# Kernel tuning notes

Measured on AMD Instinct MI355X. Metric: run time of the kernel, lower is better.

Reference implementation:

```python
import jax, jax.numpy as jnp
import numpy as np

# per-position segment id for seq_len=16: slices [0:1],[1:6],[6:9],[9:10],[10:16]
SEG = np.array([0] + [1]*5 + [2]*3 + [3] + [4]*6, dtype=np.int32)
HEAD_DIM = 3
NUM_HEADS = 2


def setup_inputs() -> dict:
    key = jax.random.key(0)
    ks = jax.random.split(key, 9)
    B = 262144
    s = 1.0 / np.sqrt(6.0)  # torch Linear init scale
    return {
        "x": jax.random.normal(ks[0], (B, 16, 6), dtype=jnp.float32),
        "Wq": jax.random.uniform(ks[1], (5, 6, 6), jnp.float32, -s, s),
        "bq": jax.random.uniform(ks[2], (5, 6), jnp.float32, -s, s),
        "Wk": jax.random.uniform(ks[3], (5, 6, 6), jnp.float32, -s, s),
        "bk": jax.random.uniform(ks[4], (5, 6), jnp.float32, -s, s),
        "Wv": jax.random.uniform(ks[5], (5, 6, 6), jnp.float32, -s, s),
        "bv": jax.random.uniform(ks[6], (5, 6), jnp.float32, -s, s),
        "Wo": jax.random.uniform(ks[7], (6, 6), jnp.float32, -s, s),
        "bo": jax.random.uniform(ks[8], (6,), jnp.float32, -s, s),
    }


def reference(x, Wq, bq, Wk, bk, Wv, bv, Wo, bo):
    B, S, D = x.shape  # S=16, D=6
    seg = jnp.asarray(SEG)

    def seg_proj(W, b):
        # torch Linear: y = x @ W.T + b; gather per-position segment weights
        return jnp.einsum('bsd,sod->bso', x, W[seg]) + b[seg]

    def heads(t):
        return t.reshape(B, S, NUM_HEADS, HEAD_DIM).transpose(0, 2, 1, 3)

    Q = heads(seg_proj(Wq, bq))  # [B,H,S,hd]
    K = heads(seg_proj(Wk, bk))
    V = heads(seg_proj(Wv, bv))

    scores = jnp.einsum('bhqd,bhkd->bhqk', Q, K) / jnp.sqrt(jnp.float32(HEAD_DIM))
    attn = jax.nn.softmax(scores, axis=-1)
    ctx = jnp.einsum('bhqk,bhkd->bhqd', attn, V)
    ctx = ctx.transpose(0, 2, 1, 3).reshape(B, S, D)
    return ctx @ Wo.T + bo
```

## Files before the change

### kernel.cpp

```cpp
#include <hip/hip_runtime.h>

#define SCALE 0.57735026918962576f

#define OFF_WQ 0
#define OFF_BQ 260
#define OFF_WK 300
#define OFF_BK 560
#define OFF_WV 600
#define OFF_BV 860
#define OFF_WO 900
#define OFF_BO 948
#define OFF_K  956
#define OFF_V  3068
#define GSTRIDE 132
#define LDS_FLOATS 5180

__global__ __launch_bounds__(256) void attn_seg_kernel(
    const float* __restrict__ x,
    const float* __restrict__ Wq, const float* __restrict__ bq,
    const float* __restrict__ Wk, const float* __restrict__ bk,
    const float* __restrict__ Wv, const float* __restrict__ bv,
    const float* __restrict__ Wo, const float* __restrict__ bo,
    float* __restrict__ out, int total)
{
    __shared__ __align__(16) float lds[LDS_FLOATS];
    const int t = threadIdx.x;

    if (t < 180) {
        unsigned sg = (unsigned)t / 36u, r = (unsigned)t - sg * 36u;
        unsigned o = r / 6u, d = r - o * 6u;
        int dst = (int)(sg * 52u + o * 8u + d);
        lds[OFF_WQ + dst] = Wq[t];
        lds[OFF_WK + dst] = Wk[t];
        lds[OFF_WV + dst] = Wv[t];
    }
    if (t < 30) {
        unsigned sg = (unsigned)t / 6u, o = (unsigned)t - sg * 6u;
        lds[OFF_BQ + sg * 8u + o] = bq[t];
        lds[OFF_BK + sg * 8u + o] = bk[t];
        lds[OFF_BV + sg * 8u + o] = bv[t];
    }
    if (t < 36) {
        unsigned o = (unsigned)t / 6u, d = (unsigned)t - o * 6u;
        lds[OFF_WO + o * 8u + d] = Wo[t];
    }
    if (t < 6) lds[OFF_BO + t] = bo[t];

    const int g = t >> 4;
    const int s = t & 15;
    const int seg = (s == 0) ? 0 : (s < 6) ? 1 : (s < 9) ? 2 : (s == 9) ? 3 : 4;

    const int pos = blockIdx.x * 256 + t;
    const bool valid = pos < total;
    float x0=0.f,x1=0.f,x2=0.f,x3=0.f,x4=0.f,x5=0.f;
    if (valid) {
        const float* xp = x + (size_t)pos * 6;
        float2 a = *(const float2*)(xp);
        float2 b = *(const float2*)(xp + 2);
        float2 c = *(const float2*)(xp + 4);
        x0=a.x; x1=a.y; x2=b.x; x3=b.y; x4=c.x; x5=c.y;
    }

    __syncthreads();

    float q[6], kk[6], vv[6];
    {
        const float* W = &lds[OFF_WQ + seg * 52];
        float4 b4 = *(const float4*)&lds[OFF_BQ + seg * 8];
        float2 b2 = *(const float2*)&lds[OFF_BQ + seg * 8 + 4];
        float bb[6] = {b4.x, b4.y, b4.z, b4.w, b2.x, b2.y};
        #pragma unroll
        for (int o = 0; o < 6; o++) {
            float4 w4 = *(const float4*)(W + o * 8);
            float2 w2 = *(const float2*)(W + o * 8 + 4);
            q[o] = bb[o] + x0*w4.x + x1*w4.y + x2*w4.z + x3*w4.w + x4*w2.x + x5*w2.y;
        }
    }
    {
        const float* W = &lds[OFF_WK + seg * 52];
        float4 b4 = *(const float4*)&lds[OFF_BK + seg * 8];
        float2 b2 = *(const float2*)&lds[OFF_BK + seg * 8 + 4];
        float bb[6] = {b4.x, b4.y, b4.z, b4.w, b2.x, b2.y};
        #pragma unroll
        for (int o = 0; o < 6; o++) {
            float4 w4 = *(const float4*)(W + o * 8);
            float2 w2 = *(const float2*)(W + o * 8 + 4);
            kk[o] = bb[o] + x0*w4.x + x1*w4.y + x2*w4.z + x3*w4.w + x4*w2.x + x5*w2.y;
        }
    }
    {
        const float* W = &lds[OFF_WV + seg * 52];
        float4 b4 = *(const float4*)&lds[OFF_BV + seg * 8];
        float2 b2 = *(const float2*)&lds[OFF_BV + seg * 8 + 4];
        float bb[6] = {b4.x, b4.y, b4.z, b4.w, b2.x, b2.y};
        #pragma unroll
        for (int o = 0; o < 6; o++) {
            float4 w4 = *(const float4*)(W + o * 8);
            float2 w2 = *(const float2*)(W + o * 8 + 4);
            vv[o] = bb[o] + x0*w4.x + x1*w4.y + x2*w4.z + x3*w4.w + x4*w2.x + x5*w2.y;
        }
    }

    {
        float* Kd = &lds[OFF_K + g * GSTRIDE + s * 8];
        *(float4*)Kd       = make_float4(kk[0], kk[1], kk[2], kk[3]);
        *(float2*)(Kd + 4) = make_float2(kk[4], kk[5]);
        float* Vd = &lds[OFF_V + g * GSTRIDE + s * 8];
        *(float4*)Vd       = make_float4(vv[0], vv[1], vv[2], vv[3]);
        *(float2*)(Vd + 4) = make_float2(vv[4], vv[5]);
    }

    __syncthreads();

    #pragma unroll
    for (int i = 0; i < 6; i++) q[i] *= SCALE;

    float sc0[16], sc1[16];
    {
        const float* Kb = &lds[OFF_K + g * GSTRIDE];
        #pragma unroll
        for (int k = 0; k < 16; k++) {
            float4 a = *(const float4*)(Kb + k * 8);
            float2 b = *(const float2*)(Kb + k * 8 + 4);
            sc0[k] = q[0]*a.x + q[1]*a.y + q[2]*a.z;
            sc1[k] = q[3]*a.w + q[4]*b.x + q[5]*b.y;
        }
    }

    float m0 = sc0[0], m1 = sc1[0];
    #pragma unroll
    for (int k = 1; k < 16; k++) { m0 = fmaxf(m0, sc0[k]); m1 = fmaxf(m1, sc1[k]); }
    float sum0 = 0.f, sum1 = 0.f;
    #pragma unroll
    for (int k = 0; k < 16; k++) {
        float e0 = __expf(sc0[k] - m0); sc0[k] = e0; sum0 += e0;
        float e1 = __expf(sc1[k] - m1); sc1[k] = e1; sum1 += e1;
    }
    const float inv0 = __builtin_amdgcn_rcpf(sum0);
    const float inv1 = __builtin_amdgcn_rcpf(sum1);

    float c0=0.f,c1=0.f,c2=0.f,c3=0.f,c4=0.f,c5=0.f;
    {
        const float* Vb = &lds[OFF_V + g * GSTRIDE];
        #pragma unroll
        for (int k = 0; k < 16; k++) {
            float4 a = *(const float4*)(Vb + k * 8);
            float2 b = *(const float2*)(Vb + k * 8 + 4);
            c0 += sc0[k]*a.x; c1 += sc0[k]*a.y; c2 += sc0[k]*a.z;
            c3 += sc1[k]*a.w; c4 += sc1[k]*b.x; c5 += sc1[k]*b.y;
        }
    }
    c0 *= inv0; c1 *= inv0; c2 *= inv0;
    c3 *= inv1; c4 *= inv1; c5 *= inv1;

    float4 bo4 = *(const float4*)&lds[OFF_BO];
    float2 bo2 = *(const float2*)&lds[OFF_BO + 4];
    float bos[6] = {bo4.x, bo4.y, bo4.z, bo4.w, bo2.x, bo2.y};
    float o_[6];
    #pragma unroll
    for (int o = 0; o < 6; o++) {
        float4 w4 = *(const float4*)&lds[OFF_WO + o * 8];
        float2 w2 = *(const float2*)&lds[OFF_WO + o * 8 + 4];
        o_[o] = bos[o] + c0*w4.x + c1*w4.y + c2*w4.z + c3*w4.w + c4*w2.x + c5*w2.y;
    }

    if (valid) {
        float* op = out + (size_t)pos * 6;
        *(float2*)(op)     = make_float2(o_[0], o_[1]);
        *(float2*)(op + 2) = make_float2(o_[2], o_[3]);
        *(float2*)(op + 4) = make_float2(o_[4], o_[5]);
    }
}

extern "C" void kernel_launch(void* const* d_in, const int* in_sizes, int n_in,
                              void* d_out, int out_size, void* d_ws, size_t ws_size,
                              hipStream_t stream) {
    const float* x  = (const float*)d_in[0];
    const float* Wq = (const float*)d_in[1];
    const float* bq = (const float*)d_in[2];
    const float* Wk = (const float*)d_in[3];
    const float* bk = (const float*)d_in[4];
    const float* Wv = (const float*)d_in[5];
    const float* bv = (const float*)d_in[6];
    const float* Wo = (const float*)d_in[7];
    const float* bo = (const float*)d_in[8];
    float* out = (float*)d_out;

    const int total = in_sizes[0] / 6;
    const int grid  = (total + 255) / 256;
    attn_seg_kernel<<<grid, 256, 0, stream>>>(x, Wq, bq, Wk, bk, Wv, bv, Wo, bo, out, total);
}
```

Baseline: 243.4 us.

## Exchange K/V across lanes with DPP row rotates instead of LDS

Replaces the LDS staging of K and V (and its barrier) with DPP row_ror moves, so each lane reads the other 15 positions' K and V straight from neighbouring lanes in its 16-lane row. The softmax is order-invariant and the PV sum pairs each rotated V with the score from the same rotation, so the result is unchanged. Biases are packed into padding slots of the weight rows so one float4 pair loads both weight and bias. This removes LDS traffic, the second __syncthreads, and most of the LDS footprint, which may raise occupancy. The cost is many DPP mov instructions.

```diff
diff --git a/kernel.cpp b/kernel.cpp
--- a/kernel.cpp
+++ b/kernel.cpp
@@ -3,17 +3,13 @@
 #define SCALE 0.57735026918962576f
 
 #define OFF_WQ 0
-#define OFF_BQ 260
-#define OFF_WK 300
-#define OFF_BK 560
-#define OFF_WV 600
-#define OFF_BV 860
-#define OFF_WO 900
-#define OFF_BO 948
-#define OFF_K  956
-#define OFF_V  3068
-#define GSTRIDE 132
-#define LDS_FLOATS 5180
+#define OFF_WK 260
+#define OFF_WV 520
+#define OFF_WO 780
+#define OFF_BO 828
+#define LDS_FLOATS 836
+
+#define ROR(v, n) __int_as_float(__builtin_amdgcn_mov_dpp(__float_as_int(v), 0x120 + (n), 0xF, 0xF, true))
 
 __global__ __launch_bounds__(256) void attn_seg_kernel(
     const float* __restrict__ x,
@@ -36,9 +32,10 @@
     }
     if (t < 30) {
         unsigned sg = (unsigned)t / 6u, o = (unsigned)t - sg * 6u;
-        lds[OFF_BQ + sg * 8u + o] = bq[t];
-        lds[OFF_BK + sg * 8u + o] = bk[t];
-        lds[OFF_BV + sg * 8u + o] = bv[t];
+        int dst = (int)(sg * 52u + o * 8u + 6u);
+        lds[OFF_WQ + dst] = bq[t];
+        lds[OFF_WK + dst] = bk[t];
+        lds[OFF_WV + dst] = bv[t];
     }
     if (t < 36) {
         unsigned o = (unsigned)t / 6u, d = (unsigned)t - o * 6u;
@@ -46,7 +43,6 @@
     }
     if (t < 6) lds[OFF_BO + t] = bo[t];
 
-    const int g = t >> 4;
     const int s = t & 15;
     const int seg = (s == 0) ? 0 : (s < 6) ? 1 : (s < 9) ? 2 : (s == 9) ? 3 : 4;
 
@@ -63,69 +59,55 @@
 
     __syncthreads();
 
-    float q[6], kk[6], vv[6];
+    float q0,q1,q2,q3,q4,q5, k0,k1,k2,k3,k4,k5, v0,v1,v2,v3,v4,v5;
     {
         const float* W = &lds[OFF_WQ + seg * 52];
-        float4 b4 = *(const float4*)&lds[OFF_BQ + seg * 8];
-        float2 b2 = *(const float2*)&lds[OFF_BQ + seg * 8 + 4];
-        float bb[6] = {b4.x, b4.y, b4.z, b4.w, b2.x, b2.y};
+        float qq[6];
         #pragma unroll
         for (int o = 0; o < 6; o++) {
-            float4 w4 = *(const float4*)(W + o * 8);
-            float2 w2 = *(const float2*)(W + o * 8 + 4);
-            q[o] = bb[o] + x0*w4.x + x1*w4.y + x2*w4.z + x3*w4.w + x4*w2.x + x5*w2.y;
+            float4 wa = *(const float4*)(W + o * 8);
+            float4 wb = *(const float4*)(W + o * 8 + 4);
+            qq[o] = wb.z + x0*wa.x + x1*wa.y + x2*wa.z + x3*wa.w + x4*wb.x + x5*wb.y;
         }
+        q0=qq[0]*SCALE; q1=qq[1]*SCALE; q2=qq[2]*SCALE;
+        q3=qq[3]*SCALE; q4=qq[4]*SCALE; q5=qq[5]*SCALE;
     }
     {
         const float* W = &lds[OFF_WK + seg * 52];
-        float4 b4 = *(const float4*)&lds[OFF_BK + seg * 8];
-        float2 b2 = *(const float2*)&lds[OFF_BK + seg * 8 + 4];
-        float bb[6] = {b4.x, b4.y, b4.z, b4.w, b2.x, b2.y};
+        float kk[6];
         #pragma unroll
         for (int o = 0; o < 6; o++) {
-            float4 w4 = *(const float4*)(W + o * 8);
-            float2 w2 = *(const float2*)(W + o * 8 + 4);
-            kk[o] = bb[o] + x0*w4.x + x1*w4.y + x2*w4.z + x3*w4.w + x4*w2.x + x5*w2.y;
+            float4 wa = *(const float4*)(W + o * 8);
+            float4 wb = *(const float4*)(W + o * 8 + 4);
+            kk[o] = wb.z + x0*wa.x + x1*wa.y + x2*wa.z + x3*wa.w + x4*wb.x + x5*wb.y;
         }
+        k0=kk[0]; k1=kk[1]; k2=kk[2]; k3=kk[3]; k4=kk[4]; k5=kk[5];
     }
     {
         const float* W = &lds[OFF_WV + seg * 52];
-        float4 b4 = *(const float4*)&lds[OFF_BV + seg * 8];
-        float2 b2 = *(const float2*)&lds[OFF_BV + seg * 8 + 4];
-        float bb[6] = {b4.x, b4.y, b4.z, b4.w, b2.x, b2.y};
+        float vv[6];
         #pragma unroll
         for (int o = 0; o < 6; o++) {
-            float4 w4 = *(const float4*)(W + o * 8);
-            float2 w2 = *(const float2*)(W + o * 8 + 4);
-            vv[o] = bb[o] + x0*w4.x + x1*w4.y + x2*w4.z + x3*w4.w + x4*w2.x + x5*w2.y;
+            float4 wa = *(const float4*)(W + o * 8);
+            float4 wb = *(const float4*)(W + o * 8 + 4);
+            vv[o] = wb.z + x0*wa.x + x1*wa.y + x2*wa.z + x3*wa.w + x4*wb.x + x5*wb.y;
         }
+        v0=vv[0]; v1=vv[1]; v2=vv[2]; v3=vv[3]; v4=vv[4]; v5=vv[5];
     }
 
-    {
-        float* Kd = &lds[OFF_K + g * GSTRIDE + s * 8];
-        *(float4*)Kd       = make_float4(kk[0], kk[1], kk[2], kk[3]);
-        *(float2*)(Kd + 4) = make_float2(kk[4], kk[5]);
-        float* Vd = &lds[OFF_V + g * GSTRIDE + s * 8];
-        *(float4*)Vd       = make_float4(vv[0], vv[1], vv[2], vv[3]);
-        *(float2*)(Vd + 4) = make_float2(vv[4], vv[5]);
-    }
-
-    __syncthreads();
-
-    #pragma unroll
-    for (int i = 0; i < 6; i++) q[i] *= SCALE;
-
     float sc0[16], sc1[16];
-    {
-        const float* Kb = &lds[OFF_K + g * GSTRIDE];
-        #pragma unroll
-        for (int k = 0; k < 16; k++) {
-            float4 a = *(const float4*)(Kb + k * 8);
-            float2 b = *(const float2*)(Kb + k * 8 + 4);
-            sc0[k] = q[0]*a.x + q[1]*a.y + q[2]*a.z;
-            sc1[k] = q[3]*a.w + q[4]*b.x + q[5]*b.y;
-        }
-    }
+    sc0[0] = q0*k0 + q1*k1 + q2*k2;
+    sc1[0] = q3*k3 + q4*k4 + q5*k5;
+    #define SCORE_STEP(J) { \
+        float a0=ROR(k0,J), a1=ROR(k1,J), a2=ROR(k2,J); \
+        float a3=ROR(k3,J), a4=ROR(k4,J), a5=ROR(k5,J); \
+        sc0[J] = q0*a0 + q1*a1 + q2*a2; \
+        sc1[J] = q3*a3 + q4*a4 + q5*a5; }
+    SCORE_STEP(1)  SCORE_STEP(2)  SCORE_STEP(3)  SCORE_STEP(4)
+    SCORE_STEP(5)  SCORE_STEP(6)  SCORE_STEP(7)  SCORE_STEP(8)
+    SCORE_STEP(9)  SCORE_STEP(10) SCORE_STEP(11) SCORE_STEP(12)
+    SCORE_STEP(13) SCORE_STEP(14) SCORE_STEP(15)
+    #undef SCORE_STEP
 
     float m0 = sc0[0], m1 = sc1[0];
     #pragma unroll
@@ -139,17 +121,20 @@
     const float inv0 = __builtin_amdgcn_rcpf(sum0);
     const float inv1 = __builtin_amdgcn_rcpf(sum1);
 
-    float c0=0.f,c1=0.f,c2=0.f,c3=0.f,c4=0.f,c5=0.f;
-    {
-        const float* Vb = &lds[OFF_V + g * GSTRIDE];
-        #pragma unroll
-        for (int k = 0; k < 16; k++) {
-            float4 a = *(const float4*)(Vb + k * 8);
-            float2 b = *(const float2*)(Vb + k * 8 + 4);
-            c0 += sc0[k]*a.x; c1 += sc0[k]*a.y; c2 += sc0[k]*a.z;
-            c3 += sc1[k]*a.w; c4 += sc1[k]*b.x; c5 += sc1[k]*b.y;
-        }
-    }
+    float c0,c1,c2,c3,c4,c5;
+    c0 = sc0[0]*v0; c1 = sc0[0]*v1; c2 = sc0[0]*v2;
+    c3 = sc1[0]*v3; c4 = sc1[0]*v4; c5 = sc1[0]*v5;
+    #define PV_STEP(J) { \
+        float b0=ROR(v0,J), b1=ROR(v1,J), b2=ROR(v2,J); \
+        float b3=ROR(v3,J), b4=ROR(v4,J), b5=ROR(v5,J); \
+        c0 += sc0[J]*b0; c1 += sc0[J]*b1; c2 += sc0[J]*b2; \
+        c3 += sc1[J]*b3; c4 += sc1[J]*b4; c5 += sc1[J]*b5; }
+    PV_STEP(1)  PV_STEP(2)  PV_STEP(3)  PV_STEP(4)
+    PV_STEP(5)  PV_STEP(6)  PV_STEP(7)  PV_STEP(8)
+    PV_STEP(9)  PV_STEP(10) PV_STEP(11) PV_STEP(12)
+    PV_STEP(13) PV_STEP(14) PV_STEP(15)
+    #undef PV_STEP
+
     c0 *= inv0; c1 *= inv0; c2 *= inv0;
     c3 *= inv1; c4 *= inv1; c5 *= inv1;
 
```

Measured after the change: 274.3 us. 1.13x slower.
